# Performance work log

Hardware: AMD Instinct MI355X
Metric: run time of the kernel (lower is better)

Reference implementation:

```python
import jax, jax.numpy as jnp
import numpy as np

H = 1024
EPS = 1e-5
MIX_SCALE = 0.1


def setup_inputs() -> dict:
    key = jax.random.key(0)
    ks = jax.random.split(key, 6)
    B, S = 8, 4096
    x = jax.random.normal(ks[0], (B, S, H), dtype=jnp.float32)
    # to_complex: Linear(H, 2H); store weight as [H, 2H] for x @ W
    W_to = jax.random.normal(ks[1], (H, 2 * H), dtype=jnp.float32) * (1.0 / np.sqrt(H))
    b_to = jax.random.normal(ks[2], (2 * H,), dtype=jnp.float32) * 0.01
    # from_complex: Linear(2H, H)
    W_from = jax.random.normal(ks[3], (2 * H, H), dtype=jnp.float32) * (1.0 / np.sqrt(2 * H))
    b_from = jax.random.normal(ks[4], (H,), dtype=jnp.float32) * 0.01
    phase_shifts = jnp.zeros((1, 1, H), dtype=jnp.float32)
    return {"x": x, "W_to": W_to, "b_to": b_to, "W_from": W_from,
            "b_from": b_from, "phase_shifts": phase_shifts}


def reference(x, W_to, b_to, W_from, b_from, phase_shifts):
    # x: [B,S,H]
    complex_repr = x @ W_to + b_to                      # [B,S,2H]
    real, imag = jnp.split(complex_repr, 2, axis=-1)    # each [B,S,H]
    magnitude = jnp.sqrt(real**2 + imag**2 + EPS)
    phase = jnp.arctan2(imag, real)                     # [B,S,H]
    # mean_j cos(phase_i - phase_j + shift)
    #   = cos(phase_i + shift) * mean_j cos(phase_j)
    #   + sin(phase_i + shift) * mean_j sin(phase_j)
    # (exact trig identity; replaces the [B,S,S,H] materialization)
    mean_cos = jnp.mean(jnp.cos(phase), axis=1, keepdims=True)  # [B,1,H]
    mean_sin = jnp.mean(jnp.sin(phase), axis=1, keepdims=True)  # [B,1,H]
    shifted = phase + phase_shifts                              # [B,S,H]
    mixed_phase = jnp.cos(shifted) * mean_cos + jnp.sin(shifted) * mean_sin
    new_phase = phase + mixed_phase * MIX_SCALE
    new_real = magnitude * jnp.cos(new_phase)
    new_imag = magnitude * jnp.sin(new_phase)
    new_complex = jnp.concatenate([new_real, new_imag], axis=-1)  # [B,S,2H]
    return new_complex @ W_from + b_from                          # [B,S,H]
```

## Files before the change

### kernel.cpp

```cpp
#include <hip/hip_runtime.h>
#include <hip/hip_bf16.h>
#include <math.h>

#define H 1024
#define N1 2048
#define BATCH 8
#define SEQ 4096
#define M_TOT (BATCH*SEQ)
#define EPS 1e-5f
#define MIX 0.1f

typedef __attribute__((ext_vector_type(8))) short bf16x8;
typedef __attribute__((ext_vector_type(4))) float f32x4;
typedef unsigned int uint_t;

static __device__ __forceinline__ float bf2f(unsigned short u) {
    return __uint_as_float(((unsigned)u) << 16);
}
static __device__ __forceinline__ unsigned short f2bf(float x) {
    __hip_bfloat16 h = __float2bfloat16(x);
    return *reinterpret_cast<unsigned short*>(&h);
}
static __device__ __forceinline__ void gload16(const void* g, void* l) {
    __builtin_amdgcn_global_load_lds(
        (const __attribute__((address_space(1))) unsigned int*)g,
        (__attribute__((address_space(3))) unsigned int*)l,
        16, 0, 0);
}
static __device__ __forceinline__ int perm2h(int c)  { return ((c & 1023) << 1) | (c >> 10); }

__global__ __launch_bounds__(256) void cvt_f32_bf16(
    const float* __restrict__ in, unsigned short* __restrict__ out, size_t n)
{
    size_t i = ((size_t)blockIdx.x * 256 + threadIdx.x) * 8;
    if (i >= n) return;
    float4 a = *(const float4*)(in + i);
    float4 b = *(const float4*)(in + i + 4);
    union { unsigned short u[8]; uint4 v; } p;
    p.u[0] = f2bf(a.x); p.u[1] = f2bf(a.y); p.u[2] = f2bf(a.z); p.u[3] = f2bf(a.w);
    p.u[4] = f2bf(b.x); p.u[5] = f2bf(b.y); p.u[6] = f2bf(b.z); p.u[7] = f2bf(b.w);
    *(uint4*)(out + i) = p.v;
}

__global__ __launch_bounds__(256) void transpose_wt(
    const float* __restrict__ in, unsigned short* __restrict__ out)
{
    __shared__ float tile[64][65];
    const int c0 = blockIdx.x * 64, r0 = blockIdx.y * 64;
    const int tc = threadIdx.x & 63, tr4 = (threadIdx.x >> 6) * 16;
    #pragma unroll
    for (int rr = 0; rr < 16; ++rr)
        tile[tr4 + rr][tc] = in[(size_t)(r0 + tr4 + rr) * N1 + c0 + tc];
    __syncthreads();
    #pragma unroll
    for (int rr = 0; rr < 16; ++rr)
        out[(size_t)perm2h(c0 + tr4 + rr) * H + r0 + tc] = f2bf(tile[tc][tr4 + rr]);
}

__global__ __launch_bounds__(256) void transpose_wf(
    const float* __restrict__ in, unsigned short* __restrict__ out)
{
    __shared__ float tile[64][65];
    const int n0 = blockIdx.x * 64, k0 = blockIdx.y * 64;
    const int tc = threadIdx.x & 63, tr4 = (threadIdx.x >> 6) * 16;
    #pragma unroll
    for (int rr = 0; rr < 16; ++rr) {
        const int k = k0 + tr4 + rr;
        tile[tr4 + rr][tc] = in[(size_t)((k >> 1) | ((k & 1) << 10)) * H + n0 + tc];
    }
    __syncthreads();
    #pragma unroll
    for (int rr = 0; rr < 16; ++rr)
        out[(size_t)(n0 + tr4 + rr) * N1 + k0 + tc] = f2bf(tile[tc][tr4 + rr]);
}

#define VM4 asm volatile("s_waitcnt vmcnt(4)" ::: "memory")
#define VM0 asm volatile("s_waitcnt vmcnt(0)" ::: "memory")

#define STG(X, BB, HH, CC, TT) \
    gload16(X##g + (size_t)((HH)*128 + (CC)*64) * KDIM + (TT)*64, \
            &X##s[BB][(HH)*8192 + (CC)*4096 + t*8])
#define STAGE_HT(X, BB, HH, TT) do { STG(X, BB, HH, 0, TT); STG(X, BB, HH, 1, TT); } while(0)

#define LDA(BB, MF, KS) (*(const bf16x8*)&As[BB][(wr*128 + (MF)*16 + fr)*64 + ((((KS)*4 + lg) ^ rsw))*8])
#define LDB(BB, NF, KS) (*(const bf16x8*)&Bs[BB][(wc*64  + (NF)*16 + fr)*64 + ((((KS)*4 + lg) ^ rsw))*8])

#define PHASE(BB, Q, STAGE_STMT, VM_STMT) do {                                  \
    if ((Q) == 0) {                                                             \
        _Pragma("unroll")                                                       \
        for (int nf = 0; nf < 4; ++nf) {                                        \
            bfr[nf][0] = LDB(BB, nf, 0);                                        \
            bfr[nf][1] = LDB(BB, nf, 1);                                        \
        }                                                                       \
    }                                                                           \
    afr[0][0] = LDA(BB, 2*(Q),   0); afr[0][1] = LDA(BB, 2*(Q),   1);           \
    afr[1][0] = LDA(BB, 2*(Q)+1, 0); afr[1][1] = LDA(BB, 2*(Q)+1, 1);           \
    STAGE_STMT;                                                                 \
    __builtin_amdgcn_s_barrier();                                               \
    asm volatile("s_waitcnt lgkmcnt(0)" ::: "memory");                          \
    __builtin_amdgcn_sched_barrier(0);                                          \
    __builtin_amdgcn_s_setprio(1);                                              \
    _Pragma("unroll")                                                           \
    for (int nf = 0; nf < 4; ++nf) {                                            \
        acc[2*(Q)][nf]   = __builtin_amdgcn_mfma_f32_16x16x32_bf16(afr[0][0], bfr[nf][0], acc[2*(Q)][nf],   0,0,0); \
        acc[2*(Q)][nf]   = __builtin_amdgcn_mfma_f32_16x16x32_bf16(afr[0][1], bfr[nf][1], acc[2*(Q)][nf],   0,0,0); \
        acc[2*(Q)+1][nf] = __builtin_amdgcn_mfma_f32_16x16x32_bf16(afr[1][0], bfr[nf][0], acc[2*(Q)+1][nf], 0,0,0); \
        acc[2*(Q)+1][nf] = __builtin_amdgcn_mfma_f32_16x16x32_bf16(afr[1][1], bfr[nf][1], acc[2*(Q)+1][nf], 0,0,0); \
    }                                                                           \
    __builtin_amdgcn_s_setprio(0);                                              \
    VM_STMT;                                                                    \
    __builtin_amdgcn_s_barrier();                                               \
} while (0)

template<int KDIM, bool G1>
__global__ __launch_bounds__(512, 2) void gemm8(
    const unsigned short* __restrict__ A,
    const unsigned short* __restrict__ Bt,
    const float* __restrict__ bias,
    void* __restrict__ Cout,
    float* __restrict__ sums)
{
    __shared__ __align__(16) unsigned short As[2][16384];
    __shared__ __align__(16) unsigned short Bs[2][16384];

    const int t    = threadIdx.x;
    const int lane = t & 63;
    const int wid  = t >> 6;
    const int wr   = wid >> 2;
    const int wc   = wid & 3;

    int m0, n0;
    if (G1) {
        const unsigned wg = ((blockIdx.x & 7) << 7) | (blockIdx.x >> 3);
        n0 = (wg & 7) * 256;
        m0 = (wg >> 3) * 256;
    } else {
        const unsigned wg = ((blockIdx.x & 7) << 6) | (blockIdx.x >> 3);
        n0 = (wg & 3) * 256;
        m0 = (wg >> 2) * 256;
    }

    const int srow = t >> 3;
    const int ssw  = srow & 7;
    const int gk   = ((t & 7) ^ ssw) * 8;
    const unsigned short* Ag = A  + (size_t)(m0 + srow) * KDIM + gk;
    const unsigned short* Bg = Bt + (size_t)(n0 + srow) * KDIM + gk;

    const int fr  = lane & 15;
    const int lg  = lane >> 4;
    const int rsw = fr & 7;

    f32x4 acc[8][4] = {};
    bf16x8 bfr[4][2];
    bf16x8 afr[2][2];

    constexpr int NITER = KDIM / 128;

    STAGE_HT(A, 0, 0, 0); STAGE_HT(A, 0, 1, 0);
    STAGE_HT(B, 0, 0, 0); STAGE_HT(B, 0, 1, 0);
    STAGE_HT(B, 1, 0, 1); STAGE_HT(B, 1, 1, 1);
    VM4;
    __builtin_amdgcn_s_barrier();

    for (int it = 0; it < NITER; ++it) {
        const int  T1   = 2 * it + 1;
        const int  T2   = 2 * it + 2;
        const int  T3   = 2 * it + 3;
        const bool more = (it + 1 < NITER);
        PHASE(0, 0, STAGE_HT(A, 1, 0, T1), );
        PHASE(0, 1, STAGE_HT(A, 1, 1, T1), );
        PHASE(0, 2, if (more) STAGE_HT(B, 0, 0, T2), );
        PHASE(0, 3, if (more) STAGE_HT(B, 0, 1, T2), if (more) { VM4; } else { VM0; });
        PHASE(1, 0, if (more) STAGE_HT(A, 0, 0, T2), );
        PHASE(1, 1, if (more) STAGE_HT(A, 0, 1, T2), );
        PHASE(1, 2, if (more) STAGE_HT(B, 1, 0, T3), );
        PHASE(1, 3, if (more) STAGE_HT(B, 1, 1, T3), if (more) { VM4; });
    }

    const int colbase = n0 + wc * 64;
    if (G1) {
        unsigned short* c1 = (unsigned short*)Cout;
        #pragma unroll
        for (int nf = 0; nf < 4; ++nf) {
            const int col = colbase + nf * 16 + fr;
            const float bb = bias[(col >> 1) | ((col & 1) << 10)];
            #pragma unroll
            for (int mf = 0; mf < 8; ++mf)
                #pragma unroll
                for (int r = 0; r < 4; ++r)
                    acc[mf][nf][r] += bb;
        }
        float lc[4] = {0, 0, 0, 0}, ls[4] = {0, 0, 0, 0};
        #pragma unroll
        for (int nf = 0; nf < 4; ++nf)
            #pragma unroll
            for (int mf = 0; mf < 8; ++mf)
                #pragma unroll
                for (int r = 0; r < 4; ++r) {
                    const float v = acc[mf][nf][r];
                    const float oth = __shfl_xor(v, 1);
                    const float re = (fr & 1) ? oth : v;
                    const float im = (fr & 1) ? v : oth;
                    const float rq = rsqrtf(fmaxf(re * re + im * im, 1e-30f));
                    lc[nf] += re * rq;
                    ls[nf] += im * rq;
                }
        #pragma unroll
        for (int nf = 0; nf < 4; ++nf) {
            lc[nf] += __shfl_xor(lc[nf], 16); lc[nf] += __shfl_xor(lc[nf], 32);
            ls[nf] += __shfl_xor(ls[nf], 16); ls[nf] += __shfl_xor(ls[nf], 32);
        }
        if (lane < 16 && !(lane & 1)) {
            const int b = m0 >> 12;
            #pragma unroll
            for (int nf = 0; nf < 4; ++nf) {
                const int hh = (colbase + nf * 16 + fr) >> 1;
                atomicAdd(&sums[(b * 2 + 0) * H + hh], lc[nf]);
                atomicAdd(&sums[(b * 2 + 1) * H + hh], ls[nf]);
            }
        }
        unsigned short* cst = &As[0][0] + wid * 2048;
        const int row16 = lane >> 2;
        #pragma unroll
        for (int mf = 0; mf < 8; ++mf) {
            #pragma unroll
            for (int nf = 0; nf < 4; ++nf)
                #pragma unroll
                for (int r = 0; r < 4; ++r)
                    cst[(lg * 4 + r) * 68 + nf * 16 + fr] = f2bf(acc[mf][nf][r]);
            const size_t grow = (size_t)(m0 + wr * 128 + mf * 16 + row16);
            #pragma unroll
            for (int c = 0; c < 2; ++c) {
                const int chunk = (lane & 3) + c * 4;
                uint4 v = *(const uint4*)&cst[row16 * 68 + chunk * 8];
                *(uint4*)&c1[grow * N1 + colbase + chunk * 8] = v;
            }
        }
    } else {
        float* o = (float*)Cout;
        #pragma unroll
        for (int nf = 0; nf < 4; ++nf) {
            const int col = colbase + nf * 16 + fr;
            const float bb = bias[col];
            #pragma unroll
            for (int mf = 0; mf < 8; ++mf) {
                #pragma unroll
                for (int r = 0; r < 4; ++r) {
                    const size_t row = (size_t)(m0 + wr * 128 + mf * 16 + lg * 4 + r);
                    o[row * H + col] = acc[mf][nf][r] + bb;
                }
            }
        }
    }
}

__global__ void finalize_pq(const float* __restrict__ sums, const float* __restrict__ ps,
                            float* __restrict__ P, float* __restrict__ Q)
{
    int i = blockIdx.x * 256 + threadIdx.x;
    int b = i >> 10, h = i & (H - 1);
    float mc = sums[(b * 2 + 0) * H + h] * (1.0f / SEQ);
    float ms = sums[(b * 2 + 1) * H + h] * (1.0f / SEQ);
    float cp = cosf(ps[h]), sp = sinf(ps[h]);
    P[i] = mc * cp + ms * sp;
    Q[i] = ms * cp - mc * sp;
}

__global__ __launch_bounds__(256) void phase_mix(
    unsigned short* __restrict__ c1, const float* __restrict__ P,
    const float* __restrict__ Q)
{
    const size_t total = (size_t)M_TOT * N1 / 8;
    for (size_t q = (size_t)blockIdx.x * 256 + threadIdx.x; q < total;
         q += (size_t)gridDim.x * 256) {
        const size_t m = q >> 8;
        const int off = ((int)q & 255) * 8;
        const int b = (int)(m >> 12);
        const int h0 = off >> 1;
        uint4* cu = (uint4*)c1;
        const size_t idx = ((size_t)m * N1 + off) >> 3;
        uint4 v = cu[idx];
        float4 Pv = *(const float4*)&P[b * H + h0];
        float4 Qv = *(const float4*)&Q[b * H + h0];
        const uint_t w[4] = { v.x, v.y, v.z, v.w };
        const float Pk[4] = { Pv.x, Pv.y, Pv.z, Pv.w };
        const float Qk[4] = { Qv.x, Qv.y, Qv.z, Qv.w };
        uint_t o[4];
        #pragma unroll
        for (int e = 0; e < 4; ++e) {
            float r  = bf2f(w[e] & 0xffff);
            float im = bf2f(w[e] >> 16);
            float tt = r * r + im * im;
            float minv = rsqrtf(fmaxf(tt, 1e-30f));
            float d = MIX * (r * Pk[e] + im * Qk[e]) * minv;
            float d2 = d * d;
            float cd = 1.0f - d2 * (0.5f - d2 * (1.0f / 24.0f));
            float sd = d * (1.0f - d2 * ((1.0f / 6.0f) - d2 * (1.0f / 120.0f)));
            float sc = sqrtf(tt + EPS) * minv;
            o[e] = (uint_t)f2bf(sc * (r * cd - im * sd))
                 | ((uint_t)f2bf(sc * (im * cd + r * sd)) << 16);
        }
        v.x = o[0]; v.y = o[1]; v.z = o[2]; v.w = o[3];
        cu[idx] = v;
    }
}

extern "C" void kernel_launch(void* const* d_in, const int* in_sizes, int n_in,
                              void* d_out, int out_size, void* d_ws, size_t ws_size,
                              hipStream_t stream) {
    const float* x  = (const float*)d_in[0];
    const float* Wt = (const float*)d_in[1];
    const float* bt = (const float*)d_in[2];
    const float* Wf = (const float*)d_in[3];
    const float* bf = (const float*)d_in[4];
    const float* ps = (const float*)d_in[5];
    float* out = (float*)d_out;

    const size_t c1_bytes   = (size_t)M_TOT * N1 * 2;
    const size_t wft_bytes  = (size_t)H * N1 * 2;
    const size_t sums_bytes = (size_t)BATCH * 2 * H * 4;
    const size_t pq_bytes   = (size_t)BATCH * H * 4;
    if (ws_size < c1_bytes + wft_bytes + sums_bytes + 2 * pq_bytes) return;

    unsigned short* c1  = (unsigned short*)d_ws;
    unsigned short* WfT = (unsigned short*)((char*)d_ws + c1_bytes);
    float* sums = (float*)((char*)d_ws + c1_bytes + wft_bytes);
    float* Pb   = (float*)((char*)d_ws + c1_bytes + wft_bytes + sums_bytes);
    float* Qb   = (float*)((char*)d_ws + c1_bytes + wft_bytes + sums_bytes + pq_bytes);

    unsigned short* xb  = (unsigned short*)d_out;
    unsigned short* WtT = (unsigned short*)d_out + (size_t)M_TOT * H;

    hipMemsetAsync(sums, 0, sums_bytes, stream);

    cvt_f32_bf16<<<dim3((unsigned)(((size_t)M_TOT * H / 8 + 255) / 256)), 256, 0, stream>>>(
        x, xb, (size_t)M_TOT * H);
    transpose_wt<<<dim3(N1 / 64, H / 64), 256, 0, stream>>>(Wt, WtT);
    transpose_wf<<<dim3(H / 64, N1 / 64), 256, 0, stream>>>(Wf, WfT);

    gemm8<H, true><<<dim3(1024), 512, 0, stream>>>(xb, WtT, bt, (void*)c1, sums);

    finalize_pq<<<dim3(BATCH * H / 256), 256, 0, stream>>>(sums, ps, Pb, Qb);
    phase_mix<<<dim3(4096), 256, 0, stream>>>(c1, Pb, Qb);

    gemm8<N1, false><<<dim3(512), 512, 0, stream>>>(c1, WfT, bf, (void*)out, nullptr);
}
```

Before: 366.7 us.

## Software-pipeline LDS fragment loads one phase ahead of MFMAs with double-buffered A regs

New measurement: 361.3 us. About the same (-1.5%).

```diff
diff --git a/kernel.cpp b/kernel.cpp
--- a/kernel.cpp
+++ b/kernel.cpp
@@ -74,8 +74,8 @@
         out[(size_t)(n0 + tr4 + rr) * N1 + k0 + tc] = f2bf(tile[tc][tr4 + rr]);
 }
 
-#define VM4 asm volatile("s_waitcnt vmcnt(4)" ::: "memory")
-#define VM0 asm volatile("s_waitcnt vmcnt(0)" ::: "memory")
+#define VMW(N) asm volatile("s_waitcnt vmcnt(" #N ")" ::: "memory")
+#define SB __builtin_amdgcn_sched_barrier(0)
 
 #define STG(X, BB, HH, CC, TT) \
     gload16(X##g + (size_t)((HH)*128 + (CC)*64) * KDIM + (TT)*64, \
@@ -85,32 +85,35 @@
 #define LDA(BB, MF, KS) (*(const bf16x8*)&As[BB][(wr*128 + (MF)*16 + fr)*64 + ((((KS)*4 + lg) ^ rsw))*8])
 #define LDB(BB, NF, KS) (*(const bf16x8*)&Bs[BB][(wc*64  + (NF)*16 + fr)*64 + ((((KS)*4 + lg) ^ rsw))*8])
 
-#define PHASE(BB, Q, STAGE_STMT, VM_STMT) do {                                  \
-    if ((Q) == 0) {                                                             \
+#define LOADB(BB, KS) do {                                                      \
+    _Pragma("unroll")                                                           \
+    for (int nf = 0; nf < 4; ++nf) bfr[nf] = LDB(BB, nf, KS); } while (0)
+#define LOADA(AN, BB, MFQ, KS) do {                                             \
+    _Pragma("unroll")                                                           \
+    for (int i = 0; i < 4; ++i) AN[i] = LDA(BB, (MFQ)*4 + i, KS); } while (0)
+#define MFMAS(AC, MFQ) do {                                                     \
+    _Pragma("unroll")                                                           \
+    for (int i = 0; i < 4; ++i)                                                 \
         _Pragma("unroll")                                                       \
-        for (int nf = 0; nf < 4; ++nf) {                                        \
-            bfr[nf][0] = LDB(BB, nf, 0);                                        \
-            bfr[nf][1] = LDB(BB, nf, 1);                                        \
-        }                                                                       \
-    }                                                                           \
-    afr[0][0] = LDA(BB, 2*(Q),   0); afr[0][1] = LDA(BB, 2*(Q),   1);           \
-    afr[1][0] = LDA(BB, 2*(Q)+1, 0); afr[1][1] = LDA(BB, 2*(Q)+1, 1);           \
-    STAGE_STMT;                                                                 \
+        for (int nf = 0; nf < 4; ++nf)                                          \
+            acc[(MFQ)*4 + i][nf] = __builtin_amdgcn_mfma_f32_16x16x32_bf16(     \
+                AC[i], bfr[nf], acc[(MFQ)*4 + i][nf], 0, 0, 0); } while (0)
+
+#define PH(VMPRE, BLOAD, ALOAD, STAGE_STMT, MFMA_STMT) do {                     \
+    VMPRE; SB;                                                                  \
+    BLOAD; SB;                                                                  \
+    ALOAD; SB;                                                                  \
+    STAGE_STMT; SB;                                                             \
     __builtin_amdgcn_s_barrier();                                               \
-    asm volatile("s_waitcnt lgkmcnt(0)" ::: "memory");                          \
-    __builtin_amdgcn_sched_barrier(0);                                          \
+    asm volatile("s_waitcnt lgkmcnt(4)" ::: "memory");                          \
+    SB;                                                                         \
     __builtin_amdgcn_s_setprio(1);                                              \
-    _Pragma("unroll")                                                           \
-    for (int nf = 0; nf < 4; ++nf) {                                            \
-        acc[2*(Q)][nf]   = __builtin_amdgcn_mfma_f32_16x16x32_bf16(afr[0][0], bfr[nf][0], acc[2*(Q)][nf],   0,0,0); \
-        acc[2*(Q)][nf]   = __builtin_amdgcn_mfma_f32_16x16x32_bf16(afr[0][1], bfr[nf][1], acc[2*(Q)][nf],   0,0,0); \
-        acc[2*(Q)+1][nf] = __builtin_amdgcn_mfma_f32_16x16x32_bf16(afr[1][0], bfr[nf][0], acc[2*(Q)+1][nf], 0,0,0); \
-        acc[2*(Q)+1][nf] = __builtin_amdgcn_mfma_f32_16x16x32_bf16(afr[1][1], bfr[nf][1], acc[2*(Q)+1][nf], 0,0,0); \
-    }                                                                           \
+    MFMA_STMT;                                                                  \
     __builtin_amdgcn_s_setprio(0);                                              \
-    VM_STMT;                                                                    \
     __builtin_amdgcn_s_barrier();                                               \
 } while (0)
+
+#define NOP ((void)0)
 
 template<int KDIM, bool G1>
 __global__ __launch_bounds__(512, 2) void gemm8(
@@ -151,30 +154,37 @@
     const int rsw = fr & 7;
 
     f32x4 acc[8][4] = {};
-    bf16x8 bfr[4][2];
-    bf16x8 afr[2][2];
+    bf16x8 bfr[4];
+    bf16x8 aX[4];
+    bf16x8 aY[4];
 
     constexpr int NITER = KDIM / 128;
 
     STAGE_HT(A, 0, 0, 0); STAGE_HT(A, 0, 1, 0);
     STAGE_HT(B, 0, 0, 0); STAGE_HT(B, 0, 1, 0);
     STAGE_HT(B, 1, 0, 1); STAGE_HT(B, 1, 1, 1);
-    VM4;
+    VMW(4);
+    SB;
     __builtin_amdgcn_s_barrier();
+    SB;
+    LOADA(aX, 0, 0, 0);
+    SB;
 
     for (int it = 0; it < NITER; ++it) {
         const int  T1   = 2 * it + 1;
         const int  T2   = 2 * it + 2;
         const int  T3   = 2 * it + 3;
         const bool more = (it + 1 < NITER);
-        PHASE(0, 0, STAGE_HT(A, 1, 0, T1), );
-        PHASE(0, 1, STAGE_HT(A, 1, 1, T1), );
-        PHASE(0, 2, if (more) STAGE_HT(B, 0, 0, T2), );
-        PHASE(0, 3, if (more) STAGE_HT(B, 0, 1, T2), if (more) { VM4; } else { VM0; });
-        PHASE(1, 0, if (more) STAGE_HT(A, 0, 0, T2), );
-        PHASE(1, 1, if (more) STAGE_HT(A, 0, 1, T2), );
-        PHASE(1, 2, if (more) STAGE_HT(B, 1, 0, T3), );
-        PHASE(1, 3, if (more) STAGE_HT(B, 1, 1, T3), if (more) { VM4; });
+        PH(NOP, LOADB(0,0), LOADA(aY,0,1,0), STAGE_HT(A,1,0,T1), MFMAS(aX,0));
+        PH(NOP, NOP, LOADA(aX,0,0,1), STAGE_HT(A,1,1,T1), MFMAS(aY,1));
+        PH(NOP, LOADB(0,1), LOADA(aY,0,1,1), if (more) STAGE_HT(B,0,0,T2), MFMAS(aX,0));
+        PH(if (more) { VMW(2); } else { VMW(0); }, NOP, LOADA(aX,1,0,0),
+           if (more) STAGE_HT(B,0,1,T2), MFMAS(aY,1));
+        PH(NOP, LOADB(1,0), LOADA(aY,1,1,0), if (more) STAGE_HT(A,0,0,T2), MFMAS(aX,0));
+        PH(NOP, NOP, LOADA(aX,1,0,1), if (more) STAGE_HT(A,0,1,T2), MFMAS(aY,1));
+        PH(NOP, LOADB(1,1), LOADA(aY,1,1,1), if (more) STAGE_HT(B,1,0,T3), MFMAS(aX,0));
+        PH(if (more) { VMW(2); }, NOP, LOADA(aX,0,0,0),
+           if (more) STAGE_HT(B,1,1,T3), MFMAS(aY,1));
     }
 
     const int colbase = n0 + wc * 64;
```
